# Optimization experiments

Measured on AMD Instinct MI355X. Metric: run time of the kernel, lower is better.

The kernel has to match this reference:

```python
import jax, jax.numpy as jnp
import numpy as np

NBINS = 256

def _equalize_flat(flat):
    # flat: [N, P] int32 pixel values in [0,255], N = B*C channels, P = H*W pixels
    N, P = flat.shape
    hist = jax.vmap(lambda v: jnp.bincount(v, length=NBINS))(flat)  # [N, 256]
    bins = jnp.arange(NBINS, dtype=jnp.int32)
    # last nonzero bin value per channel (PIL: drop last nonzero entry from the step sum)
    last_idx = jnp.max(jnp.where(hist != 0, bins[None, :], -1), axis=1)  # [N]
    last_val = jnp.take_along_axis(hist, last_idx[:, None], axis=1)[:, 0]  # [N]
    step = (P - last_val) // 255  # [N] integer floor div
    safe_step = jnp.maximum(step, 1)
    cs = jnp.cumsum(hist, axis=1)  # [N, 256]
    lut = (cs + (step // 2)[:, None]) // safe_step[:, None]
    # pad left with 0, drop last, clamp to [0,255]
    lut = jnp.concatenate([jnp.zeros((N, 1), lut.dtype), lut[:, :-1]], axis=1)
    lut = jnp.clip(lut, 0, 255)
    eq = jnp.take_along_axis(lut, flat, axis=1)  # [N, P]
    # channels with step==0 pass through unchanged
    return jnp.where((step == 0)[:, None], flat, eq)


def setup_inputs() -> dict:
    key = jax.random.key(0)
    img = jax.random.randint(key, (64, 3, 512, 512), 0, 256).astype(jnp.float32)
    return {"img": img}


def reference(img) -> jnp.ndarray:
    B, C, H, W = img.shape
    flat = img.astype(jnp.int32).reshape(B * C, H * W)
    out = _equalize_flat(flat)
    return out.reshape(B, C, H, W).astype(img.dtype)
```

## Files before the change

kernel.cpp:

```cpp
#include <hip/hip_runtime.h>


#define NBINS 256
#define BPC_H 4
#define BPC_A 16
#define NVEC_H 16384
#define NVEC_A 4096
#define NCOPY_A 16

typedef float vfloat4 __attribute__((ext_vector_type(4)));

__global__ __launch_bounds__(256) void eq_hist_pack_kernel(
    const float* __restrict__ in, unsigned int* __restrict__ pack,
    unsigned int* __restrict__ phist) {
    __shared__ unsigned int lh[NBINS * 32];
    const int t = threadIdx.x;
    const int copy = t & 31;

    for (int i = t; i < NBINS * 32; i += 256) lh[i] = 0u;
    __syncthreads();

    const size_t basev = (size_t)blockIdx.x * NVEC_H;
    const vfloat4* vin = (const vfloat4*)in + basev;
    unsigned int* pout = pack + basev;

    #pragma unroll 4
    for (int i = t; i < NVEC_H; i += 256) {
        vfloat4 v = __builtin_nontemporal_load(&vin[i]);
        int ix = min(max((int)v.x, 0), 255);
        int iy = min(max((int)v.y, 0), 255);
        int iz = min(max((int)v.z, 0), 255);
        int iw = min(max((int)v.w, 0), 255);
        atomicAdd(&lh[ix * 32 + copy], 1u);
        atomicAdd(&lh[iy * 32 + copy], 1u);
        atomicAdd(&lh[iz * 32 + copy], 1u);
        atomicAdd(&lh[iw * 32 + copy], 1u);
        pout[i] = (unsigned)ix | ((unsigned)iy << 8) |
                  ((unsigned)iz << 16) | ((unsigned)iw << 24);
    }
    __syncthreads();

    unsigned int hsum = 0;
    #pragma unroll
    for (int c = 0; c < 32; ++c) hsum += lh[t * 32 + ((t + c) & 31)];
    phist[(size_t)blockIdx.x * NBINS + t] = hsum;
}

__global__ __launch_bounds__(256, 8) void eq_lut_apply_kernel(
    const unsigned int* __restrict__ pack, const unsigned int* __restrict__ phist,
    float* __restrict__ out, int P) {
    __shared__ float slut[NBINS * NCOPY_A];
    __shared__ unsigned int s[NBINS];
    __shared__ int sidx[NBINS];
    const int t = threadIdx.x;
    const int copy = t & (NCOPY_A - 1);
    const int chan = blockIdx.x >> 4;

    unsigned int h = 0;
    const unsigned int* pb = phist + (size_t)chan * BPC_H * NBINS;
    #pragma unroll
    for (int b = 0; b < BPC_H; ++b) h += pb[b * NBINS + t];
    s[t] = h;
    sidx[t] = (h != 0u) ? t : -1;
    __syncthreads();

    for (int off = 128; off > 0; off >>= 1) {
        if (t < off) sidx[t] = max(sidx[t], sidx[t + off]);
        __syncthreads();
    }
    const int last_idx = sidx[0];
    const int last_val = (int)s[last_idx];
    const int step = (P - last_val) / 255;

    for (int off = 1; off < NBINS; off <<= 1) {
        unsigned int v = (t >= off) ? s[t - off] : 0u;
        __syncthreads();
        s[t] += v;
        __syncthreads();
    }

    float lv;
    if (step == 0) {
        lv = (float)t;
    } else {
        int csp = (t == 0) ? 0 : (int)s[t - 1];
        lv = (float)min(max((csp + (step >> 1)) / step, 0), 255);
    }
    #pragma unroll
    for (int c = 0; c < NCOPY_A; ++c)
        slut[t * NCOPY_A + ((t + c) & (NCOPY_A - 1))] = lv;
    __syncthreads();

    const size_t basev = (size_t)blockIdx.x * NVEC_A;
    const unsigned int* pin = pack + basev;
    vfloat4* vout = (vfloat4*)out + basev;

    #pragma unroll 4
    for (int i = t; i < NVEC_A; i += 256) {
        unsigned int p = pin[i];
        vfloat4 r;
        r.x = slut[(p & 255u) * NCOPY_A + copy];
        r.y = slut[((p >> 8) & 255u) * NCOPY_A + copy];
        r.z = slut[((p >> 16) & 255u) * NCOPY_A + copy];
        r.w = slut[(p >> 24) * NCOPY_A + copy];
        __builtin_nontemporal_store(r, &vout[i]);
    }
}

extern "C" void kernel_launch(void* const* d_in, const int* in_sizes, int n_in,
                              void* d_out, int out_size, void* d_ws, size_t ws_size,
                              hipStream_t stream) {
    const float* img = (const float*)d_in[0];
    float* out = (float*)d_out;

    const int P = 512 * 512;
    const int total = in_sizes[0];
    const int N = total / P;

    unsigned int* pack  = (unsigned int*)d_ws;
    unsigned int* phist = (unsigned int*)((char*)d_ws + (size_t)total);

    eq_hist_pack_kernel<<<N * BPC_H, 256, 0, stream>>>(img, pack, phist);
    eq_lut_apply_kernel<<<N * BPC_A, 256, 0, stream>>>(pack, phist, out, P);
}
```

Measured before the change: 341.8 us.

## Drop packed byte intermediate and re-read float input in apply kernel

Removes the packed 8-bit pixel buffer that the histogram kernel wrote and the apply kernel read. The apply kernel now reloads the original float image and converts it to bin indices itself. The histogram load becomes a normal cached load so the input may stay resident in the large last-level cache for the second pass. This saves one write and one read of the quarter-size intermediate, but the apply pass now reads the full float input, so DRAM traffic rises if the cache does not hold it.

Result: slower. 366.7 us (+7.3%).

```diff
diff --git a/kernel.cpp b/kernel.cpp
--- a/kernel.cpp
+++ b/kernel.cpp
@@ -10,9 +10,8 @@
 
 typedef float vfloat4 __attribute__((ext_vector_type(4)));
 
-__global__ __launch_bounds__(256) void eq_hist_pack_kernel(
-    const float* __restrict__ in, unsigned int* __restrict__ pack,
-    unsigned int* __restrict__ phist) {
+__global__ __launch_bounds__(256) void eq_hist_kernel(
+    const float* __restrict__ in, unsigned int* __restrict__ phist) {
     __shared__ unsigned int lh[NBINS * 32];
     const int t = threadIdx.x;
     const int copy = t & 31;
@@ -21,12 +20,11 @@
     __syncthreads();
 
     const size_t basev = (size_t)blockIdx.x * NVEC_H;
-    const vfloat4* vin = (const vfloat4*)in + basev;
-    unsigned int* pout = pack + basev;
+    const float4* vin = (const float4*)in + basev;
 
     #pragma unroll 4
     for (int i = t; i < NVEC_H; i += 256) {
-        vfloat4 v = __builtin_nontemporal_load(&vin[i]);
+        float4 v = vin[i];
         int ix = min(max((int)v.x, 0), 255);
         int iy = min(max((int)v.y, 0), 255);
         int iz = min(max((int)v.z, 0), 255);
@@ -35,8 +33,6 @@
         atomicAdd(&lh[iy * 32 + copy], 1u);
         atomicAdd(&lh[iz * 32 + copy], 1u);
         atomicAdd(&lh[iw * 32 + copy], 1u);
-        pout[i] = (unsigned)ix | ((unsigned)iy << 8) |
-                  ((unsigned)iz << 16) | ((unsigned)iw << 24);
     }
     __syncthreads();
 
@@ -47,7 +43,7 @@
 }
 
 __global__ __launch_bounds__(256, 8) void eq_lut_apply_kernel(
-    const unsigned int* __restrict__ pack, const unsigned int* __restrict__ phist,
+    const float* __restrict__ in, const unsigned int* __restrict__ phist,
     float* __restrict__ out, int P) {
     __shared__ float slut[NBINS * NCOPY_A];
     __shared__ unsigned int s[NBINS];
@@ -92,17 +88,17 @@
     __syncthreads();
 
     const size_t basev = (size_t)blockIdx.x * NVEC_A;
-    const unsigned int* pin = pack + basev;
+    const float4* vin = (const float4*)in + basev;
     vfloat4* vout = (vfloat4*)out + basev;
 
     #pragma unroll 4
     for (int i = t; i < NVEC_A; i += 256) {
-        unsigned int p = pin[i];
+        float4 v = vin[i];
         vfloat4 r;
-        r.x = slut[(p & 255u) * NCOPY_A + copy];
-        r.y = slut[((p >> 8) & 255u) * NCOPY_A + copy];
-        r.z = slut[((p >> 16) & 255u) * NCOPY_A + copy];
-        r.w = slut[(p >> 24) * NCOPY_A + copy];
+        r.x = slut[min(max((int)v.x, 0), 255) * NCOPY_A + copy];
+        r.y = slut[min(max((int)v.y, 0), 255) * NCOPY_A + copy];
+        r.z = slut[min(max((int)v.z, 0), 255) * NCOPY_A + copy];
+        r.w = slut[min(max((int)v.w, 0), 255) * NCOPY_A + copy];
         __builtin_nontemporal_store(r, &vout[i]);
     }
 }
@@ -117,9 +113,8 @@
     const int total = in_sizes[0];
     const int N = total / P;
 
-    unsigned int* pack  = (unsigned int*)d_ws;
-    unsigned int* phist = (unsigned int*)((char*)d_ws + (size_t)total);
+    unsigned int* phist = (unsigned int*)d_ws;
 
-    eq_hist_pack_kernel<<<N * BPC_H, 256, 0, stream>>>(img, pack, phist);
-    eq_lut_apply_kernel<<<N * BPC_A, 256, 0, stream>>>(pack, phist, out, P);
+    eq_hist_kernel<<<N * BPC_H, 256, 0, stream>>>(img, phist);
+    eq_lut_apply_kernel<<<N * BPC_A, 256, 0, stream>>>(img, phist, out, P);
 }
```
